# Optimization experiments

Hardware: AMD Instinct MI355X
Metric: run time of the kernel (lower is better)

Reference implementation:

```python
import jax, jax.numpy as jnp
import numpy as np

N = 50000      # nodes
E = 800000     # edges (avg degree 16)
IN, H, OUT = 256, 128, 64
L = 3          # num SAGEConv layers


def setup_inputs() -> dict:
    key = jax.random.key(0)
    ks = jax.random.split(key, 9)
    x = jax.random.normal(ks[0], (N, IN), dtype=jnp.float32)
    edge_index = jax.random.randint(ks[1], (2, E), 0, N, dtype=jnp.int64)
    s_in, s_h = 1.0 / np.sqrt(IN), 1.0 / np.sqrt(H)
    lin0_w = jax.random.normal(ks[2], (IN, H), dtype=jnp.float32) * s_in
    lin0_b = jnp.zeros((H,), dtype=jnp.float32)
    conv_wl = jax.random.normal(ks[3], (L, H, H), dtype=jnp.float32) * s_h  # applied to aggregated neighbors
    conv_bl = jnp.zeros((L, H), dtype=jnp.float32)
    conv_wr = jax.random.normal(ks[4], (L, H, H), dtype=jnp.float32) * s_h  # applied to root (self) features
    lin1_w = jax.random.normal(ks[5], (H, OUT), dtype=jnp.float32) * s_h
    lin1_b = jnp.zeros((OUT,), dtype=jnp.float32)
    return {"x": x, "edge_index": edge_index, "lin0_w": lin0_w, "lin0_b": lin0_b,
            "conv_wl": conv_wl, "conv_bl": conv_bl, "conv_wr": conv_wr,
            "lin1_w": lin1_w, "lin1_b": lin1_b}


def reference(x, edge_index, lin0_w, lin0_b, conv_wl, conv_bl, conv_wr, lin1_w, lin1_b):
    # Inference mode: dropout(p=0.5, training=False) is identity.
    src, dst = edge_index[0], edge_index[1]  # messages flow src -> dst (PyG source_to_target)
    deg = jax.ops.segment_sum(jnp.ones((E,), x.dtype), dst, num_segments=N)
    deg = jnp.maximum(deg, 1.0)[:, None]  # [N,1] avoid div-by-zero for isolated nodes

    h = jax.nn.relu(x @ lin0_w + lin0_b)  # [N,H]
    for i in range(L):
        # SAGEConv: lin_l(mean_agg(neighbors)) + lin_r(self)
        agg = jax.ops.segment_sum(h[src], dst, num_segments=N) / deg  # [N,H]
        h = jax.nn.relu(agg @ conv_wl[i] + conv_bl[i] + h @ conv_wr[i])
    return h @ lin1_w + lin1_b  # [N,OUT]
```

## Files before the change

### kernel.cpp

```cpp
#include <hip/hip_runtime.h>
#include <hip/hip_bf16.h>

#define N_NODES 50000
#define E_EDGES 800000
#define IN_F 256
#define H_F 128
#define OUT_F 64
#define L_LAYERS 3
#define NB_SCAN 49
#define LIN0_BLOCKS 784
#define COUNT_BLOCKS 3125
#define NPAD 50176

typedef __attribute__((ext_vector_type(8))) short bf16x8;
typedef __attribute__((ext_vector_type(4))) float f32x4;

static __device__ __forceinline__ float bf2f(unsigned short u) {
    return __uint_as_float(((unsigned int)u) << 16);
}
static __device__ __forceinline__ unsigned short f2bf(float f) {
    unsigned int b = __float_as_uint(f);
    return (unsigned short)((b + 0x7FFFu + ((b >> 16) & 1u)) >> 16);
}

__global__ __launch_bounds__(1024) void scanA_kernel(const int* __restrict__ cnt,
                                                     int* __restrict__ tmp,
                                                     int* __restrict__ bsum) {
    __shared__ int buf[1024];
    const int tid = threadIdx.x;
    const int i = blockIdx.x * 1024 + tid;
    int v = (i < N_NODES) ? cnt[(size_t)i << 4] : 0;
    buf[tid] = v;
    __syncthreads();
    for (int off = 1; off < 1024; off <<= 1) {
        int t = (tid >= off) ? buf[tid - off] : 0;
        __syncthreads();
        buf[tid] += t;
        __syncthreads();
    }
    tmp[i] = buf[tid];
    if (tid == 1023) bsum[blockIdx.x] = buf[1023];
}

__global__ void scanB_kernel(int* __restrict__ bsum) {
    int t = threadIdx.x;
    int v = (t < NB_SCAN) ? bsum[t] : 0;
    int incl = v;
    for (int off = 1; off < 64; off <<= 1) {
        int u = __shfl_up(incl, off, 64);
        if (t >= off) incl += u;
    }
    if (t < NB_SCAN) bsum[t] = incl - v;
}

__global__ __launch_bounds__(1024) void scanC_kernel(const int* __restrict__ tmp,
                                                     const int* __restrict__ bsum,
                                                     int* __restrict__ row_ptr) {
    const int i = blockIdx.x * 1024 + threadIdx.x;
    if (i < N_NODES) row_ptr[i + 1] = tmp[i] + bsum[i >> 10];
    if (i == 0) row_ptr[0] = 0;
}

__global__ void place2_kernel(const int* __restrict__ ei, const int* __restrict__ row_ptr,
                              const int* __restrict__ rank, int* __restrict__ esrc) {
    int e = blockIdx.x * blockDim.x + threadIdx.x;
    if (e < E_EDGES) {
        int s = ei[e];
        int d = ei[E_EDGES + e];
        esrc[row_ptr[d] + rank[e]] = s;
    }
}

__global__ void prep_all(const float* __restrict__ lin0_w, const float* __restrict__ conv_wl,
                         const float* __restrict__ conv_wr, const float* __restrict__ lin1_w,
                         unsigned short* __restrict__ BpL0, unsigned short* __restrict__ BpCv,
                         unsigned short* __restrict__ BpL1) {
    int gid = blockIdx.x * 256 + threadIdx.x;
    if (gid < 32768) {
        int idx = gid;
        int j = idx & 7, rest = idx >> 3;
        int c = rest & 127, gg = rest >> 7;
        BpL0[idx] = f2bf(lin0_w[(size_t)(gg * 8 + j) * 128 + c]);
    } else if (gid < 32768 + 3 * 32768) {
        int t = gid - 32768;
        int l = t >> 15, idx = t & 32767;
        int j = idx & 7, rest = idx >> 3;
        int c = rest & 127, gg = rest >> 7;
        int k = gg * 8 + j;
        const float* wl = conv_wl + (size_t)l * 16384;
        const float* wr = conv_wr + (size_t)l * 16384;
        float v = (k < 128) ? wl[(size_t)k * 128 + c] : wr[(size_t)(k - 128) * 128 + c];
        BpCv[t] = f2bf(v);
    } else if (gid < 32768 + 3 * 32768 + 8192) {
        int idx = gid - (32768 + 3 * 32768);
        int j = idx & 7, rest = idx >> 3;
        int c = rest & 63, gg = rest >> 6;
        BpL1[idx] = f2bf(lin1_w[(size_t)(gg * 8 + j) * 64 + c]);
    }
}

__global__ __launch_bounds__(256, 3) void lin0_count(
        const float* __restrict__ x, const unsigned short* __restrict__ Bp,
        const float* __restrict__ bias, unsigned short* __restrict__ hb,
        const int* __restrict__ ei, int* __restrict__ cnt, int* __restrict__ rank) {
    if (blockIdx.x < COUNT_BLOCKS) {
        int e = blockIdx.x * 256 + threadIdx.x;
        if (e < E_EDGES) {
            int d = ei[E_EDGES + e];
            rank[e] = atomicAdd(&cnt[(size_t)d << 4], 1);
        }
        return;
    }
    const int gb = blockIdx.x - COUNT_BLOCKS;
    const int tid = threadIdx.x;
    const int wave = tid >> 6, lane = tid & 63;
    const int g = lane >> 4, r = lane & 15;
    const int row_base = gb * 64 + wave * 16;
    const int row = min(row_base + r, N_NODES - 1);
    const float* xp = x + (size_t)row * IN_F + g * 8;
    float4 xv[16];
#pragma unroll
    for (int t = 0; t < 16; ++t)
        xv[t] = *(const float4*)(xp + (t >> 1) * 32 + (t & 1) * 4);
    f32x4 acc[8] = {};
#pragma unroll
    for (int kb = 0; kb < 8; ++kb) {
        const float* v0 = (const float*)&xv[kb * 2];
        bf16x8 afr;
#pragma unroll
        for (int t = 0; t < 8; ++t) afr[t] = (short)f2bf(v0[t]);
#pragma unroll
        for (int ct = 0; ct < 8; ++ct) {
            bf16x8 bfr = *(const bf16x8*)(Bp + ((size_t)(kb * 4 + g) * H_F + ct * 16 + r) * 8);
            acc[ct] = __builtin_amdgcn_mfma_f32_16x16x32_bf16(afr, bfr, acc[ct], 0, 0, 0);
        }
    }
#pragma unroll
    for (int ct = 0; ct < 8; ++ct) {
        int col = ct * 16 + r;
        float bv = bias[col];
#pragma unroll
        for (int i = 0; i < 4; ++i) {
            int orow = row_base + g * 4 + i;
            if (orow < N_NODES)
                hb[(size_t)orow * H_F + col] = f2bf(fmaxf(acc[ct][i] + bv, 0.f));
        }
    }
}

__global__ __launch_bounds__(256, 4) void conv_fused(
        const unsigned short* __restrict__ hb, const int* __restrict__ row_ptr,
        const int* __restrict__ esrc, const unsigned short* __restrict__ Bp,
        const float* __restrict__ bias, unsigned short* __restrict__ hbout) {
    __shared__ unsigned short sAgg[32 * 128];
    const int tid = threadIdx.x;
    const int wave = tid >> 6, lane = tid & 63;
    const int row0 = blockIdx.x * 32;

    {
        const int p = lane >> 4;
        const int q = lane & 15;
        for (int i = 0; i < 8; ++i) {
            const int ln = wave * 8 + i;
            const int node = row0 + ln;
            int s0 = 0, s1 = 0;
            if (node < N_NODES) { s0 = row_ptr[node]; s1 = row_ptr[node + 1]; }
            float a[8] = {};
            int j = s0;
            for (; j + 16 <= s1; j += 16) {
                int ea = esrc[j + p], eb = esrc[j + p + 4];
                int ec = esrc[j + p + 8], ed = esrc[j + p + 12];
                bf16x8 va = *(const bf16x8*)(hb + ((size_t)ea << 7) + (q << 3));
                bf16x8 vb = *(const bf16x8*)(hb + ((size_t)eb << 7) + (q << 3));
                bf16x8 vc = *(const bf16x8*)(hb + ((size_t)ec << 7) + (q << 3));
                bf16x8 vd = *(const bf16x8*)(hb + ((size_t)ed << 7) + (q << 3));
#pragma unroll
                for (int t = 0; t < 8; ++t)
                    a[t] += (bf2f((unsigned short)va[t]) + bf2f((unsigned short)vb[t])) +
                            (bf2f((unsigned short)vc[t]) + bf2f((unsigned short)vd[t]));
            }
            for (; j + 8 <= s1; j += 8) {
                int ea = esrc[j + p], eb = esrc[j + p + 4];
                bf16x8 va = *(const bf16x8*)(hb + ((size_t)ea << 7) + (q << 3));
                bf16x8 vb = *(const bf16x8*)(hb + ((size_t)eb << 7) + (q << 3));
#pragma unroll
                for (int t = 0; t < 8; ++t)
                    a[t] += bf2f((unsigned short)va[t]) + bf2f((unsigned short)vb[t]);
            }
            if (j + p < s1) {
                bf16x8 v = *(const bf16x8*)(hb + ((size_t)esrc[j + p] << 7) + (q << 3));
#pragma unroll
                for (int t = 0; t < 8; ++t) a[t] += bf2f((unsigned short)v[t]);
            }
            if (j + p + 4 < s1) {
                bf16x8 v = *(const bf16x8*)(hb + ((size_t)esrc[j + p + 4] << 7) + (q << 3));
#pragma unroll
                for (int t = 0; t < 8; ++t) a[t] += bf2f((unsigned short)v[t]);
            }
#pragma unroll
            for (int t = 0; t < 8; ++t) {
                a[t] += __shfl_xor(a[t], 16, 64);
                a[t] += __shfl_xor(a[t], 32, 64);
            }
            if (p == 0) {
                float dinv = 1.0f / (float)max(s1 - s0, 1);
                bf16x8 o;
#pragma unroll
                for (int t = 0; t < 8; ++t) o[t] = (short)f2bf(a[t] * dinv);
                int c16 = q ^ (ln & 7);
                *(bf16x8*)(sAgg + ln * 128 + (c16 << 3)) = o;
            }
        }
    }
    __syncthreads();

    const int g = lane >> 4, r = lane & 15;
    const int rt = wave & 1, ch = wave >> 1;
    const int row_base = row0 + rt * 16;
    const int srow = min(row_base + r, N_NODES - 1);
    bf16x8 sv[4];
#pragma unroll
    for (int kb = 0; kb < 4; ++kb)
        sv[kb] = *(const bf16x8*)(hb + (size_t)srow * H_F + kb * 32 + g * 8);
    f32x4 acc[4] = {};
#pragma unroll
    for (int kb = 0; kb < 8; ++kb) {
        bf16x8 afr;
        if (kb < 4) {
            int c16 = (kb * 4 + g) ^ (r & 7);
            afr = *(const bf16x8*)(sAgg + (rt * 16 + r) * 128 + (c16 << 3));
        } else {
            afr = sv[kb - 4];
        }
#pragma unroll
        for (int ct = 0; ct < 4; ++ct) {
            int col = ch * 64 + ct * 16 + r;
            bf16x8 bfr = *(const bf16x8*)(Bp + ((size_t)(kb * 4 + g) * H_F + col) * 8);
            acc[ct] = __builtin_amdgcn_mfma_f32_16x16x32_bf16(afr, bfr, acc[ct], 0, 0, 0);
        }
    }
#pragma unroll
    for (int ct = 0; ct < 4; ++ct) {
        int col = ch * 64 + ct * 16 + r;
        float bv = bias[col];
#pragma unroll
        for (int i = 0; i < 4; ++i) {
            int row = row_base + g * 4 + i;
            if (row < N_NODES)
                hbout[(size_t)row * H_F + col] = f2bf(fmaxf(acc[ct][i] + bv, 0.f));
        }
    }
}

__global__ __launch_bounds__(256, 4) void lin1_mfma(
        const unsigned short* __restrict__ hb, const unsigned short* __restrict__ Bp,
        const float* __restrict__ bias, float* __restrict__ out) {
    const int tid = threadIdx.x;
    const int wave = tid >> 6, lane = tid & 63;
    const int g = lane >> 4, r = lane & 15;
    const int row_base = blockIdx.x * 64 + wave * 16;
    const int row = min(row_base + r, N_NODES - 1);
    bf16x8 av[4];
#pragma unroll
    for (int kb = 0; kb < 4; ++kb)
        av[kb] = *(const bf16x8*)(hb + (size_t)row * H_F + kb * 32 + g * 8);
    f32x4 acc[4] = {};
#pragma unroll
    for (int kb = 0; kb < 4; ++kb) {
#pragma unroll
        for (int ct = 0; ct < 4; ++ct) {
            bf16x8 bfr = *(const bf16x8*)(Bp + ((size_t)(kb * 4 + g) * OUT_F + ct * 16 + r) * 8);
            acc[ct] = __builtin_amdgcn_mfma_f32_16x16x32_bf16(av[kb], bfr, acc[ct], 0, 0, 0);
        }
    }
#pragma unroll
    for (int ct = 0; ct < 4; ++ct) {
        int col = ct * 16 + r;
        float bv = bias[col];
#pragma unroll
        for (int i = 0; i < 4; ++i) {
            int orow = row_base + g * 4 + i;
            if (orow < N_NODES)
                out[(size_t)orow * OUT_F + col] = acc[ct][i] + bv;
        }
    }
}

extern "C" void kernel_launch(void* const* d_in, const int* in_sizes, int n_in,
                              void* d_out, int out_size, void* d_ws, size_t ws_size,
                              hipStream_t stream) {
    const float* x       = (const float*)d_in[0];
    const int*   ei      = (const int*)d_in[1];
    const float* lin0_w  = (const float*)d_in[2];
    const float* lin0_b  = (const float*)d_in[3];
    const float* conv_wl = (const float*)d_in[4];
    const float* conv_bl = (const float*)d_in[5];
    const float* conv_wr = (const float*)d_in[6];
    const float* lin1_w  = (const float*)d_in[7];
    const float* lin1_b  = (const float*)d_in[8];
    float* out = (float*)d_out;

    char* ws = (char*)d_ws;
    size_t off = 0;
    auto alloc = [&](size_t bytes) {
        void* p = ws + off;
        off = (off + bytes + 255) & ~(size_t)255;
        return p;
    };
    int* cnt     = (int*)alloc((size_t)N_NODES * 16 * 4);
    int* row_ptr = (int*)alloc((size_t)(N_NODES + 1) * 4);
    int* esrc    = (int*)alloc((size_t)E_EDGES * 4);
    int* rank    = (int*)alloc((size_t)E_EDGES * 4);
    int* tmp     = (int*)alloc((size_t)NB_SCAN * 1024 * 4);
    int* bsum    = (int*)alloc(64 * 4);
    unsigned short* hb0  = (unsigned short*)alloc((size_t)NPAD * H_F * 2);
    unsigned short* hb1  = (unsigned short*)alloc((size_t)NPAD * H_F * 2);
    unsigned short* BpL0 = (unsigned short*)alloc((size_t)IN_F * H_F * 2);
    unsigned short* BpCv = (unsigned short*)alloc((size_t)L_LAYERS * 256 * H_F * 2);
    unsigned short* BpL1 = (unsigned short*)alloc((size_t)H_F * OUT_F * 2);

    hipMemsetAsync(cnt, 0, (size_t)N_NODES * 16 * 4, stream);
    prep_all<<<544, 256, 0, stream>>>(lin0_w, conv_wl, conv_wr, lin1_w, BpL0, BpCv, BpL1);

    lin0_count<<<COUNT_BLOCKS + LIN0_BLOCKS, 256, 0, stream>>>(
        x, BpL0, lin0_b, hb0, ei, cnt, rank);

    scanA_kernel<<<NB_SCAN, 1024, 0, stream>>>(cnt, tmp, bsum);
    scanB_kernel<<<1, 64, 0, stream>>>(bsum);
    scanC_kernel<<<NB_SCAN, 1024, 0, stream>>>(tmp, bsum, row_ptr);
    place2_kernel<<<COUNT_BLOCKS, 256, 0, stream>>>(ei, row_ptr, rank, esrc);

    unsigned short* h = hb0;
    unsigned short* nh = hb1;
    for (int l = 0; l < L_LAYERS; ++l) {
        conv_fused<<<NPAD / 32, 256, 0, stream>>>(h, row_ptr, esrc,
                                                  BpCv + (size_t)l * 256 * H_F,
                                                  conv_bl + (size_t)l * H_F, nh);
        unsigned short* t = h; h = nh; nh = t;
    }

    lin1_mfma<<<NPAD / 64, 256, 0, stream>>>(h, BpL1, lin1_b, out);
}
```

Baseline: 310.8 us.

## Fold edge counting into lin0 blocks and halve conv block size

The lin0 kernel no longer launches separate counting blocks. Each lin0 thread now issues the atomics for four edges up front, strided by the grid size, and writes their ranks after the MFMA work, so the atomic latency can overlap the GEMM. The x tile is no longer held in 16 float4 registers; it is loaded per k-step, which frees registers for higher occupancy. The conv kernel now uses 16-row, 128-thread blocks with 8 blocks per CU instead of 32-row, 256-thread blocks, which gives finer scheduling over the irregular gathers. The trade-off is that the conv weights are reloaded by twice as many blocks.

```diff
diff --git a/kernel.cpp b/kernel.cpp
--- a/kernel.cpp
+++ b/kernel.cpp
@@ -9,7 +9,7 @@
 #define L_LAYERS 3
 #define NB_SCAN 49
 #define LIN0_BLOCKS 784
-#define COUNT_BLOCKS 3125
+#define E_STRIDE 200704
 #define NPAD 50176
 
 typedef __attribute__((ext_vector_type(8))) short bf16x8;
@@ -99,36 +99,40 @@
     }
 }
 
-__global__ __launch_bounds__(256, 3) void lin0_count(
+__global__ __launch_bounds__(256, 4) void lin0_count(
         const float* __restrict__ x, const unsigned short* __restrict__ Bp,
         const float* __restrict__ bias, unsigned short* __restrict__ hb,
         const int* __restrict__ ei, int* __restrict__ cnt, int* __restrict__ rank) {
-    if (blockIdx.x < COUNT_BLOCKS) {
-        int e = blockIdx.x * 256 + threadIdx.x;
-        if (e < E_EDGES) {
+    const int tid = threadIdx.x;
+    const int gtid = blockIdx.x * 256 + tid;
+
+    int rk[4];
+    bool val[4];
+#pragma unroll
+    for (int k = 0; k < 4; ++k) {
+        int e = gtid + k * E_STRIDE;
+        val[k] = (e < E_EDGES);
+        if (val[k]) {
             int d = ei[E_EDGES + e];
-            rank[e] = atomicAdd(&cnt[(size_t)d << 4], 1);
-        }
-        return;
-    }
-    const int gb = blockIdx.x - COUNT_BLOCKS;
-    const int tid = threadIdx.x;
+            rk[k] = atomicAdd(&cnt[(size_t)d << 4], 1);
+        }
+    }
+
     const int wave = tid >> 6, lane = tid & 63;
     const int g = lane >> 4, r = lane & 15;
-    const int row_base = gb * 64 + wave * 16;
+    const int row_base = blockIdx.x * 64 + wave * 16;
     const int row = min(row_base + r, N_NODES - 1);
     const float* xp = x + (size_t)row * IN_F + g * 8;
-    float4 xv[16];
-#pragma unroll
-    for (int t = 0; t < 16; ++t)
-        xv[t] = *(const float4*)(xp + (t >> 1) * 32 + (t & 1) * 4);
     f32x4 acc[8] = {};
 #pragma unroll
     for (int kb = 0; kb < 8; ++kb) {
-        const float* v0 = (const float*)&xv[kb * 2];
+        float4 v0 = *(const float4*)(xp + kb * 32);
+        float4 v1 = *(const float4*)(xp + kb * 32 + 4);
         bf16x8 afr;
-#pragma unroll
-        for (int t = 0; t < 8; ++t) afr[t] = (short)f2bf(v0[t]);
+        afr[0] = (short)f2bf(v0.x); afr[1] = (short)f2bf(v0.y);
+        afr[2] = (short)f2bf(v0.z); afr[3] = (short)f2bf(v0.w);
+        afr[4] = (short)f2bf(v1.x); afr[5] = (short)f2bf(v1.y);
+        afr[6] = (short)f2bf(v1.z); afr[7] = (short)f2bf(v1.w);
 #pragma unroll
         for (int ct = 0; ct < 8; ++ct) {
             bf16x8 bfr = *(const bf16x8*)(Bp + ((size_t)(kb * 4 + g) * H_F + ct * 16 + r) * 8);
@@ -146,16 +150,20 @@
                 hb[(size_t)orow * H_F + col] = f2bf(fmaxf(acc[ct][i] + bv, 0.f));
         }
     }
-}
-
-__global__ __launch_bounds__(256, 4) void conv_fused(
+
+#pragma unroll
+    for (int k = 0; k < 4; ++k)
+        if (val[k]) rank[gtid + k * E_STRIDE] = rk[k];
+}
+
+__global__ __launch_bounds__(128, 8) void conv_fused(
         const unsigned short* __restrict__ hb, const int* __restrict__ row_ptr,
         const int* __restrict__ esrc, const unsigned short* __restrict__ Bp,
         const float* __restrict__ bias, unsigned short* __restrict__ hbout) {
-    __shared__ unsigned short sAgg[32 * 128];
+    __shared__ unsigned short sAgg[16 * 128];
     const int tid = threadIdx.x;
     const int wave = tid >> 6, lane = tid & 63;
-    const int row0 = blockIdx.x * 32;
+    const int row0 = blockIdx.x * 16;
 
     {
         const int p = lane >> 4;
@@ -215,9 +223,8 @@
     __syncthreads();
 
     const int g = lane >> 4, r = lane & 15;
-    const int rt = wave & 1, ch = wave >> 1;
-    const int row_base = row0 + rt * 16;
-    const int srow = min(row_base + r, N_NODES - 1);
+    const int ch = wave;
+    const int srow = min(row0 + r, N_NODES - 1);
     bf16x8 sv[4];
 #pragma unroll
     for (int kb = 0; kb < 4; ++kb)
@@ -228,7 +235,7 @@
         bf16x8 afr;
         if (kb < 4) {
             int c16 = (kb * 4 + g) ^ (r & 7);
-            afr = *(const bf16x8*)(sAgg + (rt * 16 + r) * 128 + (c16 << 3));
+            afr = *(const bf16x8*)(sAgg + r * 128 + (c16 << 3));
         } else {
             afr = sv[kb - 4];
         }
@@ -245,7 +252,7 @@
         float bv = bias[col];
 #pragma unroll
         for (int i = 0; i < 4; ++i) {
-            int row = row_base + g * 4 + i;
+            int row = row0 + g * 4 + i;
             if (row < N_NODES)
                 hbout[(size_t)row * H_F + col] = f2bf(fmaxf(acc[ct][i] + bv, 0.f));
         }
@@ -322,18 +329,17 @@
     hipMemsetAsync(cnt, 0, (size_t)N_NODES * 16 * 4, stream);
     prep_all<<<544, 256, 0, stream>>>(lin0_w, conv_wl, conv_wr, lin1_w, BpL0, BpCv, BpL1);
 
-    lin0_count<<<COUNT_BLOCKS + LIN0_BLOCKS, 256, 0, stream>>>(
-        x, BpL0, lin0_b, hb0, ei, cnt, rank);
+    lin0_count<<<LIN0_BLOCKS, 256, 0, stream>>>(x, BpL0, lin0_b, hb0, ei, cnt, rank);
 
     scanA_kernel<<<NB_SCAN, 1024, 0, stream>>>(cnt, tmp, bsum);
     scanB_kernel<<<1, 64, 0, stream>>>(bsum);
     scanC_kernel<<<NB_SCAN, 1024, 0, stream>>>(tmp, bsum, row_ptr);
-    place2_kernel<<<COUNT_BLOCKS, 256, 0, stream>>>(ei, row_ptr, rank, esrc);
+    place2_kernel<<<(E_EDGES + 255) / 256, 256, 0, stream>>>(ei, row_ptr, rank, esrc);
 
     unsigned short* h = hb0;
     unsigned short* nh = hb1;
     for (int l = 0; l < L_LAYERS; ++l) {
-        conv_fused<<<NPAD / 32, 256, 0, stream>>>(h, row_ptr, esrc,
+        conv_fused<<<NPAD / 16, 128, 0, stream>>>(h, row_ptr, esrc,
                                                   BpCv + (size_t)l * 256 * H_F,
                                                   conv_bl + (size_t)l * H_F, nh);
         unsigned short* t = h; h = nh; nh = t;
```

Result: faster. 299.5 us (-3.6%).
